# Performance work log

Measured on AMD Instinct MI355X. Metric: run time of the kernel, lower is better.

The kernel has to match this reference:

```python
import jax, jax.numpy as jnp
import numpy as np

LEAK = 0.1
LOG_2PI = float(np.log(2.0 * np.pi))


def setup_inputs() -> dict:
    key = jax.random.key(0)
    k1, k2, k3, k4 = jax.random.split(key, 4)
    B, S, K = 128, 8192, 16
    obvs = jax.random.normal(k1, (B, S, 1), dtype=jnp.float32)
    mu = jax.random.normal(k2, (K,), dtype=jnp.float32)
    log_sigma = 0.1 * jax.random.normal(k3, (K,), dtype=jnp.float32)
    prior_logits = jax.random.normal(k4, (K,), dtype=jnp.float32)
    return {"obvs": obvs, "mu": mu, "log_sigma": log_sigma, "prior_logits": prior_logits}


def _log_transition(num_states: int) -> jnp.ndarray:
    # LeakyTransfer: diagonal-dominant stochastic matrix, stay prob 1-leak,
    # leak mass spread uniformly over the other K-1 states.
    eye = jnp.eye(num_states, dtype=jnp.float32)
    A = (1.0 - LEAK) * eye + (LEAK / (num_states - 1)) * (1.0 - eye)
    return jnp.log(A)


def reference(obvs, mu, log_sigma, prior_logits):
    K = mu.shape[0]
    # Gaussian emission NLL per state: [B, S, K]
    sigma = jnp.exp(log_sigma)
    nll = 0.5 * ((obvs - mu) / sigma) ** 2 + log_sigma + 0.5 * LOG_2PI
    ln_em = -nll  # ln_emission_probs

    log_prior = jax.nn.log_softmax(prior_logits)  # CategoricalPrior
    logA = _log_transition(K)  # [K, K] (from -> to)

    # forward recursion: carry[b, j] = ln_em[b, t, j] + logsumexp_i(carry[b, i] + logA[i, j])
    init = ln_em[:, 0, :] + log_prior  # [B, K]
    em_rest = jnp.swapaxes(ln_em[:, 1:, :], 0, 1)  # [S-1, B, K]

    def step(carry, em_t):
        trans = jax.nn.logsumexp(carry[:, :, None] + logA[None, :, :], axis=1)  # [B, K]
        carry = em_t + trans
        return carry, None

    final, _ = jax.lax.scan(step, init, em_rest)
    return jnp.sum(jax.nn.logsumexp(final, axis=-1))
```

## Files before the change

### kernel.cpp

```cpp
#include <hip/hip_runtime.h>

#define NB 128
#define NS 8192
#define NC 256
#define NCP 16
#define NL (NS / NC)
#define M4 (NL / 4)

#define LOG2E 1.4426950408889634f
#define HLOG2PI 0.918938533204672742f
#define LN2 0.69314718055994531f

#define ROWS 20
#define UNIT 320

typedef float v2f __attribute__((ext_vector_type(2)));

__device__ __forceinline__ float fexp2(float x) { return __builtin_amdgcn_exp2f(x); }
__device__ __forceinline__ float flog2(float x) { return __builtin_amdgcn_logf(x); }

__device__ __forceinline__ float gsum16(float v) {
    v += __shfl_xor(v, 1, 16);
    v += __shfl_xor(v, 2, 16);
    v += __shfl_xor(v, 4, 16);
    v += __shfl_xor(v, 8, 16);
    return v;
}
__device__ __forceinline__ float gmax16(float v) {
    v = fmaxf(v, __shfl_xor(v, 1, 16));
    v = fmaxf(v, __shfl_xor(v, 2, 16));
    v = fmaxf(v, __shfl_xor(v, 4, 16));
    v = fmaxf(v, __shfl_xor(v, 8, 16));
    return v;
}

template <int K>
__device__ __forceinline__ int rotk(int x) {
    return __builtin_amdgcn_mov_dpp(x, 0x120 + K, 0xF, 0xF, true);
}

__device__ __forceinline__ float step2(v2f (&Wv)[8], float T, float xx,
                                       float A2, float B2, float C2) {
    const float amb = 0.9f - 0.1f / 15.0f;
    const float bco = 0.1f / 15.0f;
    float myl = fexp2(fmaf(xx, fmaf(xx, A2, B2), C2));
    int mi = __float_as_int(myl);
    float bT = bco * T;
    v2f bT2 = {bT, bT};
    v2f amb2 = {amb, amb};
    v2f L0 = {myl,                          __int_as_float(rotk<1>(mi))};
    v2f L1 = {__int_as_float(rotk<2>(mi)),  __int_as_float(rotk<3>(mi))};
    v2f L2 = {__int_as_float(rotk<4>(mi)),  __int_as_float(rotk<5>(mi))};
    v2f L3 = {__int_as_float(rotk<6>(mi)),  __int_as_float(rotk<7>(mi))};
    v2f L4 = {__int_as_float(rotk<8>(mi)),  __int_as_float(rotk<9>(mi))};
    v2f L5 = {__int_as_float(rotk<10>(mi)), __int_as_float(rotk<11>(mi))};
    v2f L6 = {__int_as_float(rotk<12>(mi)), __int_as_float(rotk<13>(mi))};
    v2f L7 = {__int_as_float(rotk<14>(mi)), __int_as_float(rotk<15>(mi))};
    Wv[0] = __builtin_elementwise_fma(amb2, Wv[0], bT2) * L0;
    Wv[1] = __builtin_elementwise_fma(amb2, Wv[1], bT2) * L1;
    Wv[2] = __builtin_elementwise_fma(amb2, Wv[2], bT2) * L2;
    Wv[3] = __builtin_elementwise_fma(amb2, Wv[3], bT2) * L3;
    Wv[4] = __builtin_elementwise_fma(amb2, Wv[4], bT2) * L4;
    Wv[5] = __builtin_elementwise_fma(amb2, Wv[5], bT2) * L5;
    Wv[6] = __builtin_elementwise_fma(amb2, Wv[6], bT2) * L6;
    Wv[7] = __builtin_elementwise_fma(amb2, Wv[7], bT2) * L7;
    v2f s = ((Wv[0] + Wv[1]) + (Wv[2] + Wv[3])) + ((Wv[4] + Wv[5]) + (Wv[6] + Wv[7]));
    return s.x + s.y;
}

__device__ __forceinline__ void combineUnits(float* lds, int ua, int ub, int ud, int lane) {
    const float* MbR = lds + ub * UNIT;
    const float* MaR = lds + ua * UNIT;
    float mxa = lds[ua * UNIT + 16];
    float mxb = lds[ub * UNIT + 16];
    int a = lane >> 3, cc = lane & 7;
    float b0[16], b1[16];
    const float4* pb0 = (const float4*)(MbR + (2 * a) * ROWS);
    const float4* pb1 = (const float4*)(MbR + (2 * a + 1) * ROWS);
#pragma unroll
    for (int q = 0; q < 4; ++q) {
        *(float4*)&b0[4 * q] = pb0[q];
        *(float4*)&b1[4 * q] = pb1[q];
    }
    float c00 = 0.f, c01 = 0.f, c10 = 0.f, c11 = 0.f;
#pragma unroll
    for (int k = 0; k < 16; ++k) {
        float2 av = *(const float2*)(MaR + k * ROWS + 2 * cc);
        c00 = fmaf(b0[k], av.x, c00);
        c01 = fmaf(b0[k], av.y, c01);
        c10 = fmaf(b1[k], av.x, c10);
        c11 = fmaf(b1[k], av.y, c11);
    }
    float cs0 = c00 + c10;
    float cs1 = c01 + c11;
    cs0 += __shfl_xor(cs0, 8);  cs1 += __shfl_xor(cs1, 8);
    cs0 += __shfl_xor(cs0, 16); cs1 += __shfl_xor(cs1, 16);
    cs0 += __shfl_xor(cs0, 32); cs1 += __shfl_xor(cs1, 32);
    float mxc = fmaxf(cs0, cs1);
    mxc = fmaxf(mxc, __shfl_xor(mxc, 1));
    mxc = fmaxf(mxc, __shfl_xor(mxc, 2));
    mxc = fmaxf(mxc, __shfl_xor(mxc, 4));
    float is = 1.0f / mxc;
    c00 *= is; c01 *= is; c10 *= is; c11 *= is;
    float* dR = lds + ud * UNIT;
    *(float2*)(dR + (2 * a) * ROWS + 2 * cc)     = make_float2(c00, c01);
    *(float2*)(dR + (2 * a + 1) * ROWS + 2 * cc) = make_float2(c10, c11);
    if (lane == 0) lds[ud * UNIT + 16] = mxa + mxb + flog2(mxc);
}

__global__ __launch_bounds__(256, 6) void hmm_phase1(const float* __restrict__ obvs,
                                                     const float* __restrict__ mu,
                                                     const float* __restrict__ log_sigma,
                                                     float* __restrict__ wsW,
                                                     float* __restrict__ wsM,
                                                     float* __restrict__ out) {
    __shared__ float lds[16 * UNIT];
    int tid = blockIdx.x * 256 + threadIdx.x;
    if (tid == 0) out[0] = 0.0f;
    int r = threadIdx.x & 15;
    int u = threadIdx.x >> 4;
    int g = tid >> 4;
    int b = g >> 8;
    int c = g & (NC - 1);

    float ls = log_sigma[r];
    float mk = mu[r];
    float iv = fexp2(-2.0f * LOG2E * ls);
    float A2 = -0.5f * LOG2E * iv;
    float B2 = LOG2E * mk * iv;
    float C2 = LOG2E * (-0.5f * mk * mk * iv - ls - HLOG2PI);

    v2f Wv[8];
#pragma unroll
    for (int i = 0; i < 8; ++i) Wv[i] = (v2f){0.0f, 0.0f};
    Wv[0].x = 1.0f;
    int ilog = 0;
    float T = 1.0f;

    const float4* ob4 = (const float4*)(obvs + (long)b * NS) + c * M4;
    float4 xv = ob4[0];
    float4 xn = ob4[1];
    if (c) T = step2(Wv, T, xv.x, A2, B2, C2);
    T = step2(Wv, T, xv.y, A2, B2, C2);
    T = step2(Wv, T, xv.z, A2, B2, C2);
    T = step2(Wv, T, xv.w, A2, B2, C2);
    {
        int te = (__float_as_int(T) >> 23) & 255;
        int ok = (te != 0);
        float s = ok ? __int_as_float((254 - te) << 23) : 1.0f;
        ilog += ok ? (te - 127) : 0;
        v2f s2 = {s, s};
#pragma unroll
        for (int i = 0; i < 8; ++i) Wv[i] *= s2;
        T *= s;
    }
    xv = xn;
    for (int m = 1; m < M4; ++m) {
        xn = ob4[(m + 1) < M4 ? (m + 1) : m];
        T = step2(Wv, T, xv.x, A2, B2, C2);
        T = step2(Wv, T, xv.y, A2, B2, C2);
        T = step2(Wv, T, xv.z, A2, B2, C2);
        T = step2(Wv, T, xv.w, A2, B2, C2);
        int te = (__float_as_int(T) >> 23) & 255;
        int ok = (te != 0);
        float s = ok ? __int_as_float((254 - te) << 23) : 1.0f;
        ilog += ok ? (te - 127) : 0;
        v2f s2 = {s, s};
#pragma unroll
        for (int i = 0; i < 8; ++i) Wv[i] *= s2;
        T *= s;
        xv = xn;
    }

    float lg = (float)ilog + flog2(T);
    float mx = gmax16(lg);
    float sc = fexp2((float)ilog - mx);

    float* Ru = lds + u * UNIT;
#pragma unroll
    for (int i = 0; i < 8; ++i) {
        int j0 = (r + 2 * i) & 15;
        int j1 = (r + 2 * i + 1) & 15;
        Ru[j0 * ROWS + r] = Wv[i].x * sc;
        Ru[j1 * ROWS + r] = Wv[i].y * sc;
    }
    if (r == 0) Ru[16] = mx;
    __syncthreads();

    int lane = threadIdx.x & 63;
    int wid = threadIdx.x >> 6;
#pragma unroll
    for (int q = 0; q < 2; ++q) {
        int p = 2 * wid + q;
        combineUnits(lds, 2 * p, 2 * p + 1, 2 * p, lane);
    }
    __syncthreads();
    if (wid < 4) combineUnits(lds, 4 * wid, 4 * wid + 2, 4 * wid, lane);
    __syncthreads();
    if (wid < 2) combineUnits(lds, 8 * wid, 8 * wid + 4, 8 * wid, lane);
    __syncthreads();
    if (wid == 0) combineUnits(lds, 0, 8, 0, lane);
    __syncthreads();

    wsW[(long)blockIdx.x * 256 + threadIdx.x] =
        lds[(threadIdx.x >> 4) * ROWS + (threadIdx.x & 15)];
    if (threadIdx.x == 0) wsM[blockIdx.x] = lds[16];
}

__global__ __launch_bounds__(256, 2) void hmm_phase23(const float* __restrict__ obvs,
                                                      const float* __restrict__ mu,
                                                      const float* __restrict__ log_sigma,
                                                      const float* __restrict__ prior_logits,
                                                      const float* __restrict__ wsW,
                                                      const float* __restrict__ wsM,
                                                      float* __restrict__ out) {
    __shared__ float lds[16 * UNIT];
    int bb = blockIdx.x;
    int tid = threadIdx.x;
    int wid = tid >> 6;
    int lane = tid & 63;

    const float4* src = (const float4*)(wsW + (long)bb * NCP * 256);
#pragma unroll
    for (int q = 0; q < 4; ++q) {
        int f = tid + q * 256;
        float4 v = src[f];
        int m = f >> 6, idx = f & 63, j = idx >> 2, kq = idx & 3;
        *(float4*)(lds + m * UNIT + j * ROWS + kq * 4) = v;
    }
    if (tid < 16) lds[tid * UNIT + 16] = 0.0f;
    __syncthreads();

#pragma unroll
    for (int q = 0; q < 2; ++q) {
        int p = 2 * wid + q;
        combineUnits(lds, 2 * p, 2 * p + 1, 2 * p, lane);
    }
    __syncthreads();
    if (wid < 4) combineUnits(lds, 4 * wid, 4 * wid + 2, 4 * wid, lane);
    __syncthreads();
    if (wid < 2) combineUnits(lds, 8 * wid, 8 * wid + 4, 8 * wid, lane);
    __syncthreads();
    if (wid == 0) combineUnits(lds, 0, 8, 0, lane);
    __syncthreads();

    if (tid < 16) {
        int jj = tid;
        float ls = log_sigma[jj];
        float mk = mu[jj];
        float iv = fexp2(-2.0f * LOG2E * ls);
        float A2 = -0.5f * LOG2E * iv;
        float B2 = LOG2E * mk * iv;
        float C2 = LOG2E * (-0.5f * mk * mk * iv - ls - HLOG2PI);
        float x = obvs[(long)bb * NS];
        float e = fexp2(LOG2E * prior_logits[jj]);
        float Z = gsum16(e);
        float p0 = fexp2(fmaf(x, fmaf(x, A2, B2), C2)) * e;
        const float* Mrow = lds + jj * ROWS;
        float mr[16];
        *(float4*)&mr[0]  = ((const float4*)Mrow)[0];
        *(float4*)&mr[4]  = ((const float4*)Mrow)[1];
        *(float4*)&mr[8]  = ((const float4*)Mrow)[2];
        *(float4*)&mr[12] = ((const float4*)Mrow)[3];
        float q = 0.0f;
#pragma unroll
        for (int rr = 0; rr < 16; ++rr) q = fmaf(mr[rr], __shfl(p0, rr, 16), q);
        float Tq = gsum16(q);
        float pm = wsM[bb * NCP + jj];
        float msum = gsum16(pm);
        if (jj == 0) {
            float res = (flog2(Tq) + lds[16] - flog2(Z) + msum) * LN2;
            atomicAdd(out, res);
        }
    }
}

extern "C" void kernel_launch(void* const* d_in, const int* in_sizes, int n_in,
                              void* d_out, int out_size, void* d_ws, size_t ws_size,
                              hipStream_t stream) {
    const float* obvs = (const float*)d_in[0];
    const float* mu = (const float*)d_in[1];
    const float* log_sigma = (const float*)d_in[2];
    const float* prior_logits = (const float*)d_in[3];
    float* out = (float*)d_out;

    float* wsW = (float*)d_ws;
    float* wsM = wsW + (size_t)NB * NCP * 256;

    hmm_phase1<<<dim3(NB * NC * 16 / 256), dim3(256), 0, stream>>>(obvs, mu, log_sigma,
                                                                   wsW, wsM, out);
    hmm_phase23<<<dim3(NB), dim3(256), 0, stream>>>(obvs, mu, log_sigma, prior_logits,
                                                    wsW, wsM, out);
}
```

Before: 95.80 us.

## Halve sequence chunks per batch and fuse DPP rotation into multiply

Reduces the number of sequence chunks per batch from 256 to 128, so each thread group walks twice as many timesteps and the second phase combines 8 partial matrices instead of 16. The inner step drops packed v2f math and uses inline-asm v_mul_f32_dpp with row_ror, so each rotated emission is fused into its multiply instead of needing separate DPP moves. This cuts per-step instruction count and reduction work. In exchange there are half as many threads, a longer serial chain per thread, and a lower occupancy hint (launch bounds 6 to 4), so latency hiding may suffer.

Result: faster. 92.55 us (-3.4%).

```diff
diff --git a/kernel.cpp b/kernel.cpp
--- a/kernel.cpp
+++ b/kernel.cpp
@@ -2,8 +2,8 @@
 
 #define NB 128
 #define NS 8192
-#define NC 256
-#define NCP 16
+#define NC 128
+#define NCP 8
 #define NL (NS / NC)
 #define M4 (NL / 4)
 
@@ -13,8 +13,6 @@
 
 #define ROWS 20
 #define UNIT 320
-
-typedef float v2f __attribute__((ext_vector_type(2)));
 
 __device__ __forceinline__ float fexp2(float x) { return __builtin_amdgcn_exp2f(x); }
 __device__ __forceinline__ float flog2(float x) { return __builtin_amdgcn_logf(x); }
@@ -34,38 +32,32 @@
     return v;
 }
 
-template <int K>
-__device__ __forceinline__ int rotk(int x) {
-    return __builtin_amdgcn_mov_dpp(x, 0x120 + K, 0xF, 0xF, true);
-}
-
-__device__ __forceinline__ float step2(v2f (&Wv)[8], float T, float xx,
+#define MULROT(w, K)                                                            \
+    asm("v_mul_f32_dpp %0, %1, %0 row_ror:" #K " row_mask:0xf bank_mask:0xf"    \
+        : "+v"(w) : "v"(mylg))
+
+__device__ __forceinline__ float stepS(float (&W)[16], float T, float xx,
                                        float A2, float B2, float C2) {
     const float amb = 0.9f - 0.1f / 15.0f;
     const float bco = 0.1f / 15.0f;
     float myl = fexp2(fmaf(xx, fmaf(xx, A2, B2), C2));
-    int mi = __float_as_int(myl);
     float bT = bco * T;
-    v2f bT2 = {bT, bT};
-    v2f amb2 = {amb, amb};
-    v2f L0 = {myl,                          __int_as_float(rotk<1>(mi))};
-    v2f L1 = {__int_as_float(rotk<2>(mi)),  __int_as_float(rotk<3>(mi))};
-    v2f L2 = {__int_as_float(rotk<4>(mi)),  __int_as_float(rotk<5>(mi))};
-    v2f L3 = {__int_as_float(rotk<6>(mi)),  __int_as_float(rotk<7>(mi))};
-    v2f L4 = {__int_as_float(rotk<8>(mi)),  __int_as_float(rotk<9>(mi))};
-    v2f L5 = {__int_as_float(rotk<10>(mi)), __int_as_float(rotk<11>(mi))};
-    v2f L6 = {__int_as_float(rotk<12>(mi)), __int_as_float(rotk<13>(mi))};
-    v2f L7 = {__int_as_float(rotk<14>(mi)), __int_as_float(rotk<15>(mi))};
-    Wv[0] = __builtin_elementwise_fma(amb2, Wv[0], bT2) * L0;
-    Wv[1] = __builtin_elementwise_fma(amb2, Wv[1], bT2) * L1;
-    Wv[2] = __builtin_elementwise_fma(amb2, Wv[2], bT2) * L2;
-    Wv[3] = __builtin_elementwise_fma(amb2, Wv[3], bT2) * L3;
-    Wv[4] = __builtin_elementwise_fma(amb2, Wv[4], bT2) * L4;
-    Wv[5] = __builtin_elementwise_fma(amb2, Wv[5], bT2) * L5;
-    Wv[6] = __builtin_elementwise_fma(amb2, Wv[6], bT2) * L6;
-    Wv[7] = __builtin_elementwise_fma(amb2, Wv[7], bT2) * L7;
-    v2f s = ((Wv[0] + Wv[1]) + (Wv[2] + Wv[3])) + ((Wv[4] + Wv[5]) + (Wv[6] + Wv[7]));
-    return s.x + s.y;
+    float mylg;
+    asm("v_mov_b32 %0, %1\n\ts_nop 1" : "=v"(mylg) : "v"(myl));
+#pragma unroll
+    for (int k = 0; k < 16; ++k) W[k] = fmaf(amb, W[k], bT);
+    W[0] *= myl;
+    MULROT(W[1], 1);   MULROT(W[2], 2);   MULROT(W[3], 3);
+    MULROT(W[4], 4);   MULROT(W[5], 5);   MULROT(W[6], 6);
+    MULROT(W[7], 7);   MULROT(W[8], 8);   MULROT(W[9], 9);
+    MULROT(W[10], 10); MULROT(W[11], 11); MULROT(W[12], 12);
+    MULROT(W[13], 13); MULROT(W[14], 14); MULROT(W[15], 15);
+    float a0 = W[0] + W[1],   a1 = W[2] + W[3];
+    float a2 = W[4] + W[5],   a3 = W[6] + W[7];
+    float a4 = W[8] + W[9],   a5 = W[10] + W[11];
+    float a6 = W[12] + W[13], a7 = W[14] + W[15];
+    float b0 = a0 + a1, b1 = a2 + a3, b2 = a4 + a5, b3 = a6 + a7;
+    return (b0 + b1) + (b2 + b3);
 }
 
 __device__ __forceinline__ void combineUnits(float* lds, int ua, int ub, int ud, int lane) {
@@ -108,7 +100,7 @@
     if (lane == 0) lds[ud * UNIT + 16] = mxa + mxb + flog2(mxc);
 }
 
-__global__ __launch_bounds__(256, 6) void hmm_phase1(const float* __restrict__ obvs,
+__global__ __launch_bounds__(256, 4) void hmm_phase1(const float* __restrict__ obvs,
                                                      const float* __restrict__ mu,
                                                      const float* __restrict__ log_sigma,
                                                      float* __restrict__ wsW,
@@ -120,7 +112,7 @@
     int r = threadIdx.x & 15;
     int u = threadIdx.x >> 4;
     int g = tid >> 4;
-    int b = g >> 8;
+    int b = g >> 7;
     int c = g & (NC - 1);
 
     float ls = log_sigma[r];
@@ -130,44 +122,42 @@
     float B2 = LOG2E * mk * iv;
     float C2 = LOG2E * (-0.5f * mk * mk * iv - ls - HLOG2PI);
 
-    v2f Wv[8];
-#pragma unroll
-    for (int i = 0; i < 8; ++i) Wv[i] = (v2f){0.0f, 0.0f};
-    Wv[0].x = 1.0f;
+    float W[16];
+#pragma unroll
+    for (int i = 0; i < 16; ++i) W[i] = 0.0f;
+    W[0] = 1.0f;
     int ilog = 0;
     float T = 1.0f;
 
     const float4* ob4 = (const float4*)(obvs + (long)b * NS) + c * M4;
     float4 xv = ob4[0];
     float4 xn = ob4[1];
-    if (c) T = step2(Wv, T, xv.x, A2, B2, C2);
-    T = step2(Wv, T, xv.y, A2, B2, C2);
-    T = step2(Wv, T, xv.z, A2, B2, C2);
-    T = step2(Wv, T, xv.w, A2, B2, C2);
+    if (c) T = stepS(W, T, xv.x, A2, B2, C2);
+    T = stepS(W, T, xv.y, A2, B2, C2);
+    T = stepS(W, T, xv.z, A2, B2, C2);
+    T = stepS(W, T, xv.w, A2, B2, C2);
     {
         int te = (__float_as_int(T) >> 23) & 255;
         int ok = (te != 0);
         float s = ok ? __int_as_float((254 - te) << 23) : 1.0f;
         ilog += ok ? (te - 127) : 0;
-        v2f s2 = {s, s};
-#pragma unroll
-        for (int i = 0; i < 8; ++i) Wv[i] *= s2;
+#pragma unroll
+        for (int i = 0; i < 16; ++i) W[i] *= s;
         T *= s;
     }
     xv = xn;
     for (int m = 1; m < M4; ++m) {
         xn = ob4[(m + 1) < M4 ? (m + 1) : m];
-        T = step2(Wv, T, xv.x, A2, B2, C2);
-        T = step2(Wv, T, xv.y, A2, B2, C2);
-        T = step2(Wv, T, xv.z, A2, B2, C2);
-        T = step2(Wv, T, xv.w, A2, B2, C2);
+        T = stepS(W, T, xv.x, A2, B2, C2);
+        T = stepS(W, T, xv.y, A2, B2, C2);
+        T = stepS(W, T, xv.z, A2, B2, C2);
+        T = stepS(W, T, xv.w, A2, B2, C2);
         int te = (__float_as_int(T) >> 23) & 255;
         int ok = (te != 0);
         float s = ok ? __int_as_float((254 - te) << 23) : 1.0f;
         ilog += ok ? (te - 127) : 0;
-        v2f s2 = {s, s};
-#pragma unroll
-        for (int i = 0; i < 8; ++i) Wv[i] *= s2;
+#pragma unroll
+        for (int i = 0; i < 16; ++i) W[i] *= s;
         T *= s;
         xv = xn;
     }
@@ -178,11 +168,9 @@
 
     float* Ru = lds + u * UNIT;
 #pragma unroll
-    for (int i = 0; i < 8; ++i) {
-        int j0 = (r + 2 * i) & 15;
-        int j1 = (r + 2 * i + 1) & 15;
-        Ru[j0 * ROWS + r] = Wv[i].x * sc;
-        Ru[j1 * ROWS + r] = Wv[i].y * sc;
+    for (int k = 0; k < 16; ++k) {
+        int j = (r + k) & 15;
+        Ru[j * ROWS + r] = W[k] * sc;
     }
     if (r == 0) Ru[16] = mx;
     __syncthreads();
@@ -222,26 +210,20 @@
 
     const float4* src = (const float4*)(wsW + (long)bb * NCP * 256);
 #pragma unroll
-    for (int q = 0; q < 4; ++q) {
+    for (int q = 0; q < 2; ++q) {
         int f = tid + q * 256;
         float4 v = src[f];
         int m = f >> 6, idx = f & 63, j = idx >> 2, kq = idx & 3;
         *(float4*)(lds + m * UNIT + j * ROWS + kq * 4) = v;
     }
-    if (tid < 16) lds[tid * UNIT + 16] = 0.0f;
-    __syncthreads();
-
-#pragma unroll
-    for (int q = 0; q < 2; ++q) {
-        int p = 2 * wid + q;
-        combineUnits(lds, 2 * p, 2 * p + 1, 2 * p, lane);
-    }
-    __syncthreads();
-    if (wid < 4) combineUnits(lds, 4 * wid, 4 * wid + 2, 4 * wid, lane);
-    __syncthreads();
-    if (wid < 2) combineUnits(lds, 8 * wid, 8 * wid + 4, 8 * wid, lane);
-    __syncthreads();
-    if (wid == 0) combineUnits(lds, 0, 8, 0, lane);
+    if (tid < NCP) lds[tid * UNIT + 16] = 0.0f;
+    __syncthreads();
+
+    if (wid < 4) combineUnits(lds, 2 * wid, 2 * wid + 1, 2 * wid, lane);
+    __syncthreads();
+    if (wid < 2) combineUnits(lds, 4 * wid, 4 * wid + 2, 4 * wid, lane);
+    __syncthreads();
+    if (wid == 0) combineUnits(lds, 0, 4, 0, lane);
     __syncthreads();
 
     if (tid < 16) {
@@ -266,7 +248,7 @@
 #pragma unroll
         for (int rr = 0; rr < 16; ++rr) q = fmaf(mr[rr], __shfl(p0, rr, 16), q);
         float Tq = gsum16(q);
-        float pm = wsM[bb * NCP + jj];
+        float pm = (jj < NCP) ? wsM[bb * NCP + jj] : 0.0f;
         float msum = gsum16(pm);
         if (jj == 0) {
             float res = (flog2(Tq) + lds[16] - flog2(Z) + msum) * LN2;
```
